# Kernel optimization log

Measured on AMD Instinct MI355X. Metric: run time of the kernel, lower is better.

## Reference

```python
import jax, jax.numpy as jnp
import numpy as np

B, T, D, P = 4, 2048, 1024, 128

def setup_inputs() -> dict:
    key = jax.random.key(0)
    ks = jax.random.split(key, 10)
    inp = {
        "x": jax.random.normal(ks[0], (B, T, D), dtype=jnp.float32),
        "Q_filt": jax.random.normal(ks[1], (P, P), dtype=jnp.float32),
        "K_filt": jax.random.normal(ks[2], (P, P), dtype=jnp.float32),
        "W_in": jax.random.normal(ks[3], (D, P), dtype=jnp.float32) / np.sqrt(D),
        "b_in": jax.random.normal(ks[4], (P,), dtype=jnp.float32) * 0.01,
        "W_v": jax.random.normal(ks[5], (D, P), dtype=jnp.float32) / np.sqrt(D),
        "b_v": jax.random.normal(ks[6], (P,), dtype=jnp.float32) * 0.01,
        "W_o": jax.random.normal(ks[7], (P, D), dtype=jnp.float32) / np.sqrt(P),
        "b_o": jax.random.normal(ks[8], (D,), dtype=jnp.float32) * 0.01,
        "decay": jnp.ones((T,), dtype=jnp.float32),
    }
    return inp

def reference(x, Q_filt, K_filt, W_in, b_in, W_v, b_v, W_o, b_o, decay):
    # x: (B,T,D)
    x_proj = x @ W_in + b_in          # (B,T,P)
    Q = x_proj @ Q_filt               # (B,T,P)
    K = x_proj @ K_filt               # (B,T,P)
    V = x @ W_v + b_v                 # (B,T,P)
    # outer-product state per timestep, scaled by per-step decay
    Z = jnp.einsum('bti,btj->btij', V, K) * decay[None, :, None, None]
    H = jnp.cumsum(Z, axis=1)         # (B,T,P,P) cumulative linear-attn state
    Y = jnp.einsum('bti,btij->btj', Q, H)  # (B,T,P)
    return Y @ W_o + b_o              # (B,T,D)
```

## Files before the change

### kernel.cpp

```cpp
#include <hip/hip_runtime.h>

#define BB 4
#define TT 2048
#define DD 1024
#define PP 128
#define NC 16
#define CH 128

typedef __attribute__((ext_vector_type(8))) short bf16x8;
typedef __attribute__((ext_vector_type(4))) float f32x4;

__device__ inline ushort f2bf(float f) {
  unsigned u = __builtin_bit_cast(unsigned, f);
  u = (u + 0x7FFF + ((u >> 16) & 1)) >> 16;
  return (ushort)u;
}

__device__ inline void gll16(const void* g, void* l) {
  __builtin_amdgcn_global_load_lds(
      (const __attribute__((address_space(1))) void*)g,
      (__attribute__((address_space(3))) void*)l, 16, 0, 0);
}

__device__ inline int swzoff(int row, int kbyte) {
  return row * 256 + (kbyte ^ ((row & 7) << 4));
}
__device__ inline int swz128(int row, int kbyte) {
  return row * 128 + (kbyte ^ ((row & 7) << 4));
}

template <int NI, int NT>
__device__ inline void stage_swz(const ushort* __restrict__ g, int ld, int koff,
                                 char* lds, int tid) {
#pragma unroll
  for (int j = 0; j < NI; ++j) {
    int L = j * (NT * 16) + tid * 16;
    int row = L >> 8;
    int off = (L & 255) ^ ((row & 7) << 4);
    gll16(g + (size_t)row * ld + koff + (off >> 1),
          lds + j * (NT * 16) + ((tid & (NT - 64)) << 4));
  }
}
template <int NI, int NT>
__device__ inline void stage_swz128(const ushort* __restrict__ g, int ld,
                                    int koff, char* lds, int tid) {
#pragma unroll
  for (int j = 0; j < NI; ++j) {
    int L = j * (NT * 16) + tid * 16;
    int row = L >> 7;
    int off = (L & 127) ^ ((row & 7) << 4);
    gll16(g + (size_t)row * ld + koff + (off >> 1),
          lds + j * (NT * 16) + ((tid & (NT - 64)) << 4));
  }
}

__device__ inline bf16x8 ld_swz(const char* lds, int row, int kbyte) {
  return *(const bf16x8*)(lds + swzoff(row, kbyte));
}
__device__ inline bf16x8 ld_swz128(const char* lds, int row, int kbyte) {
  return *(const bf16x8*)(lds + swz128(row, kbyte));
}

__device__ inline bf16x8 pack8(const float4& a, const float4& b) {
  bf16x8 v;
  v[0] = (short)f2bf(a.x); v[1] = (short)f2bf(a.y);
  v[2] = (short)f2bf(a.z); v[3] = (short)f2bf(a.w);
  v[4] = (short)f2bf(b.x); v[5] = (short)f2bf(b.y);
  v[6] = (short)f2bf(b.z); v[7] = (short)f2bf(b.w);
  return v;
}

__global__ __launch_bounds__(256) void prep_t(
    const float* __restrict__ Qf, const float* __restrict__ Kf,
    const float* __restrict__ W_in, const float* __restrict__ b_in,
    const float* __restrict__ W_v, const float* __restrict__ b_v,
    const float* __restrict__ W_o, ushort* __restrict__ WcatT,
    ushort* __restrict__ QKcT, ushort* __restrict__ WoT,
    float* __restrict__ bcat) {
  const int bid = blockIdx.x;
  const int t = threadIdx.x;
  if (bid == 104) {
    bcat[t] = (t < 128) ? b_in[t] : b_v[t - 128];
    return;
  }
  const float* src;
  ushort* dst;
  int ld_src, ld_dst, nn0;
  if (bid < 64) {
    int tn = bid >> 4, tk = bid & 15;
    src = (tn < 2) ? W_in : W_v;
    nn0 = (tn & 1) * 64;
    ld_src = 128;
    src += (size_t)(tk * 64) * 128;
    dst = WcatT + (size_t)(tn * 64) * 1024 + tk * 64;
    ld_dst = 1024;
  } else if (bid < 96) {
    int j = bid - 64, tn = j >> 1, tk = j & 1;
    src = W_o;
    nn0 = tn * 64;
    ld_src = 1024;
    src += (size_t)(tk * 64) * 1024;
    dst = WoT + (size_t)(tn * 64) * 128 + tk * 64;
    ld_dst = 128;
  } else {
    int j = bid - 96, tn = j >> 1, tk = j & 1;
    src = (tn < 2) ? Qf : Kf;
    nn0 = (tn & 1) * 64;
    ld_src = 128;
    src += (size_t)(tk * 64) * 128;
    dst = QKcT + (size_t)(tn * 64) * 128 + tk * 64;
    ld_dst = 128;
  }
  __shared__ ushort Tt[64][68];
  const int kr = t >> 4, nc = (t & 15) * 4;
#pragma unroll
  for (int p = 0; p < 4; ++p) {
    float4 v = *(const float4*)&src[(size_t)(p * 16 + kr) * ld_src + nn0 + nc];
    Tt[p * 16 + kr][nc + 0] = f2bf(v.x);
    Tt[p * 16 + kr][nc + 1] = f2bf(v.y);
    Tt[p * 16 + kr][nc + 2] = f2bf(v.z);
    Tt[p * 16 + kr][nc + 3] = f2bf(v.w);
  }
  __syncthreads();
  const int nr = t >> 4, kc = (t & 15) * 4;
#pragma unroll
  for (int p = 0; p < 4; ++p) {
    ushort4 o;
    o.x = Tt[kc + 0][p * 16 + nr];
    o.y = Tt[kc + 1][p * 16 + nr];
    o.z = Tt[kc + 2][p * 16 + nr];
    o.w = Tt[kc + 3][p * 16 + nr];
    *(ushort4*)&dst[(size_t)(p * 16 + nr) * ld_dst + kc] = o;
  }
}

__global__ __launch_bounds__(512, 4) void gemm_xw(
    const float* __restrict__ x, const ushort* __restrict__ WcatT,
    const float* __restrict__ bcat, ushort* __restrict__ XP,
    ushort* __restrict__ V, ushort* __restrict__ VT) {
  __shared__ char sm[2][24576];
  const int bid = blockIdx.x;
  const int swz = (bid & 7) * 32 + (bid >> 3);
  const int bm = (swz >> 1) * 64;
  const int bn = (swz & 1) * 128;
  const int tid = threadIdx.x, w = tid >> 6, l = tid & 63;
  const int wr = w >> 2, wc = w & 3, lr = l & 15, lk = l >> 4;

  const int arow = tid >> 3;
  const int acol = (tid & 7) * 8;
  const float* Ax = x + (size_t)(bm + arow) * DD + acol;
  const ushort* Bg = WcatT + (size_t)bn * DD;

  float4 ra[2];
  f32x4 z = {0.f, 0.f, 0.f, 0.f};
  f32x4 acc[2][2];
#pragma unroll
  for (int m = 0; m < 2; ++m)
#pragma unroll
    for (int n = 0; n < 2; ++n) acc[m][n] = z;

#define LOADA(t)                                                 \
  {                                                              \
    const float4* p = (const float4*)(Ax + (((t) & 15) << 6));   \
    ra[0] = p[0];                                                \
    ra[1] = p[1];                                                \
  }
#define WRITEA(lds) \
  { *(bf16x8*)((lds) + swz128(arow, acol * 2)) = pack8(ra[0], ra[1]); }

  LOADA(0);
  stage_swz128<2, 512>(Bg, DD, 0, sm[0] + 8192, tid);
  asm volatile("s_waitcnt vmcnt(2)" ::: "memory");
  WRITEA(sm[0]);
  LOADA(1);

  int cur = 0;
  for (int t = 0; t < 16; ++t) {
    char* nxt = sm[cur ^ 1];
    stage_swz128<2, 512>(Bg, DD, ((t + 1) & 15) << 6, nxt + 8192, tid);
    asm volatile("s_waitcnt vmcnt(2)" ::: "memory");
    WRITEA(nxt);
    LOADA(t + 2);
    asm volatile("s_waitcnt lgkmcnt(0)" ::: "memory");
    __builtin_amdgcn_s_barrier();
    const char* cp = sm[cur];
#pragma unroll
    for (int ks = 0; ks < 2; ++ks) {
      const int kb = ks * 64 + lk * 16;
      bf16x8 af[2], bfp[2];
#pragma unroll
      for (int m = 0; m < 2; ++m)
        af[m] = ld_swz128(cp, wr * 32 + m * 16 + lr, kb);
#pragma unroll
      for (int n = 0; n < 2; ++n)
        bfp[n] = ld_swz128(cp + 8192, wc * 32 + n * 16 + lr, kb);
#pragma unroll
      for (int m = 0; m < 2; ++m)
#pragma unroll
        for (int n = 0; n < 2; ++n)
          acc[m][n] = __builtin_amdgcn_mfma_f32_16x16x32_bf16(af[m], bfp[n], acc[m][n], 0, 0, 0);
    }
    __builtin_amdgcn_s_barrier();
    cur ^= 1;
  }
  asm volatile("s_waitcnt vmcnt(0)" ::: "memory");
#undef LOADA
#undef WRITEA

  if (bn == 0) {
#pragma unroll
    for (int m = 0; m < 2; ++m)
#pragma unroll
      for (int n = 0; n < 2; ++n) {
        const int rowb = bm + wr * 32 + m * 16 + lk * 4;
        const int col = wc * 32 + n * 16 + lr;
        const float bv = bcat[col];
#pragma unroll
        for (int j = 0; j < 4; ++j)
          XP[(size_t)(rowb + j) * PP + col] = f2bf(acc[m][n][j] + bv);
      }
  } else {
    ushort(*VTt)[72] = (ushort(*)[72]) & sm[0][0];
#pragma unroll
    for (int m = 0; m < 2; ++m)
#pragma unroll
      for (int n = 0; n < 2; ++n) {
        const int tl = wr * 32 + m * 16 + lk * 4;
        const int cc = wc * 32 + n * 16 + lr;
        const float bv = bcat[128 + cc];
#pragma unroll
        for (int j = 0; j < 4; ++j) {
          ushort u = f2bf(acc[m][n][j] + bv);
          V[(size_t)(bm + tl + j) * PP + cc] = u;
          VTt[cc][tl + j] = u;
        }
      }
    __syncthreads();
    const int row = tid >> 2;
#pragma unroll
    for (int i = 0; i < 2; ++i) {
      const int ch = (tid & 3) * 2 + i;
      bf16x8 v = *(const bf16x8*)&VTt[row][ch * 8];
      *(bf16x8*)&VT[(size_t)row * (BB * TT) + bm + ch * 8] = v;
    }
  }
}

__global__ __launch_bounds__(512, 4) void qk_state(
    const ushort* __restrict__ XP, const ushort* __restrict__ QKcT,
    const ushort* __restrict__ VT, const float* __restrict__ decay,
    ushort* __restrict__ Qb, ushort* __restrict__ KdT,
    float* __restrict__ Sc2) {
  __shared__ char sm[81920];
  char* smA = sm;
  char* smB = sm + 16384;
  const int blk = blockIdx.x;
  const int bc = blk >> 1, mh = blk & 1;
  const size_t r0 = (size_t)(bc >> 4) * TT + (bc & 15) * CH;
  const size_t rh = r0 + mh * 64;
  const int tid = threadIdx.x, w = tid >> 6, l = tid & 63;
  const int wr = w >> 2, wc = w & 3, lr = l & 15, lk = l >> 4;

  stage_swz<2, 512>(XP + rh * PP, PP, 0, smA, tid);
  stage_swz<8, 512>(QKcT, PP, 0, smB, tid);

  f32x4 z = {0.f, 0.f, 0.f, 0.f};
  f32x4 acc[2][4];
#pragma unroll
  for (int m = 0; m < 2; ++m)
#pragma unroll
    for (int n = 0; n < 4; ++n) acc[m][n] = z;
  __syncthreads();

#pragma unroll
  for (int ks = 0; ks < 4; ++ks) {
    const int kb = ks * 64 + lk * 16;
    bf16x8 af[2], bfp[4];
#pragma unroll
    for (int m = 0; m < 2; ++m) af[m] = ld_swz(smA, wr * 32 + m * 16 + lr, kb);
#pragma unroll
    for (int n = 0; n < 4; ++n)
      bfp[n] = ld_swz(smB, wc * 64 + n * 16 + lr, kb);
#pragma unroll
    for (int m = 0; m < 2; ++m)
#pragma unroll
      for (int n = 0; n < 4; ++n)
        acc[m][n] = __builtin_amdgcn_mfma_f32_16x16x32_bf16(af[m], bfp[n], acc[m][n], 0, 0, 0);
  }
  __syncthreads();

#pragma unroll
  for (int m = 0; m < 2; ++m)
#pragma unroll
    for (int n = 0; n < 4; ++n) {
      const int rowl = wr * 32 + m * 16 + lk * 4;
      const int col = wc * 64 + n * 16 + lr;
      if (col < 128) {
#pragma unroll
        for (int j = 0; j < 4; ++j)
          Qb[(rh + rowl + j) * PP + col] = f2bf(acc[m][n][j]);
      } else {
        const int cc = col - 128;
#pragma unroll
        for (int j = 0; j < 4; ++j) {
          float v = acc[m][n][j] * decay[(rh + rowl + j) & (TT - 1)];
          *(ushort*)(smA + swz128(cc, (rowl + j) * 2)) = f2bf(v);
        }
      }
    }
  __syncthreads();

  {
    const int cc = tid >> 2;
#pragma unroll
    for (int i = 0; i < 2; ++i) {
      const int ch = (tid & 3) * 2 + i;
      bf16x8 v = ld_swz128(smA, cc, ch * 16);
      *(bf16x8*)&KdT[(size_t)cc * (BB * TT) + rh + ch * 8] = v;
    }
  }

  f32x4 a2[4][2];
#pragma unroll
  for (int m = 0; m < 4; ++m)
#pragma unroll
    for (int n = 0; n < 2; ++n) a2[m][n] = z;
#pragma unroll
  for (int ks = 0; ks < 2; ++ks) {
    const int kb = ks * 64 + lk * 16;
    const int kk = ks * 32 + lk * 8;
    bf16x8 af[4], bfp[2];
#pragma unroll
    for (int m = 0; m < 4; ++m)
      af[m] = ld_swz128(smA, wr * 64 + m * 16 + lr, kb);
#pragma unroll
    for (int n = 0; n < 2; ++n)
      bfp[n] = *(const bf16x8*)&VT[(size_t)(wc * 32 + n * 16 + lr) * (BB * TT) + rh + kk];
#pragma unroll
    for (int m = 0; m < 4; ++m)
#pragma unroll
      for (int n = 0; n < 2; ++n)
        a2[m][n] = __builtin_amdgcn_mfma_f32_16x16x32_bf16(af[m], bfp[n], a2[m][n], 0, 0, 0);
  }
#pragma unroll
  for (int m = 0; m < 4; ++m)
#pragma unroll
    for (int n = 0; n < 2; ++n)
#pragma unroll
      for (int j = 0; j < 4; ++j)
        Sc2[((size_t)bc * 2 + mh) * 16384 +
            (size_t)(wr * 64 + m * 16 + lk * 4 + j) * 128 +
            (wc * 32 + n * 16 + lr)] = a2[m][n][j];
}

__global__ __launch_bounds__(256) void chunk_scan(const float* __restrict__ Sc2,
                                                  ushort* __restrict__ SxT) {
  const int b = blockIdx.y;
  const int e = blockIdx.x * 256 + threadIdx.x;
  float run = 0.f;
#pragma unroll
  for (int c = 0; c < NC; ++c) {
    const size_t bc = (size_t)(b * NC + c);
    SxT[bc * 16384 + e] = f2bf(run);
    run += Sc2[bc * 2 * 16384 + e] + Sc2[(bc * 2 + 1) * 16384 + e];
  }
}

__global__ __launch_bounds__(256) void attn_mfma(
    const ushort* __restrict__ Qb, const ushort* __restrict__ V,
    const ushort* __restrict__ KdT, const ushort* __restrict__ SxT,
    ushort* __restrict__ Y) {
  __shared__ char Am[64 * 256];
  const int blk = blockIdx.x;
  const int bc = blk >> 2, hr = (blk >> 1) & 1, hc = blk & 1;
  const int b = bc >> 4, c = bc & 15;
  const size_t r0 = (size_t)b * TT + c * CH;
  const int tid = threadIdx.x, w = tid >> 6, l = tid & 63;
  const int wr = w >> 1, wc = w & 1, lr = l & 15, lk = l >> 4;

  f32x4 z = {0.f, 0.f, 0.f, 0.f};
  f32x4 a1[2][4];
#pragma unroll
  for (int m = 0; m < 2; ++m)
#pragma unroll
    for (int n = 0; n < 4; ++n) a1[m][n] = z;

#pragma unroll
  for (int ks = 0; ks < 4; ++ks) {
    const int kk = ks * 32 + lk * 8;
    bf16x8 af[2], bf[4];
#pragma unroll
    for (int m = 0; m < 2; ++m)
      af[m] = *(const bf16x8*)&Qb[(r0 + hr * 64 + wr * 32 + m * 16 + lr) * 128 + kk];
#pragma unroll
    for (int n = 0; n < 4; ++n)
      bf[n] = *(const bf16x8*)&V[(r0 + wc * 64 + n * 16 + lr) * 128 + kk];
#pragma unroll
    for (int m = 0; m < 2; ++m)
#pragma unroll
      for (int n = 0; n < 4; ++n)
        a1[m][n] = __builtin_amdgcn_mfma_f32_16x16x32_bf16(af[m], bf[n], a1[m][n], 0, 0, 0);
  }
#pragma unroll
  for (int m = 0; m < 2; ++m)
#pragma unroll
    for (int n = 0; n < 4; ++n)
#pragma unroll
      for (int j = 0; j < 4; ++j) {
        int tl = wr * 32 + m * 16 + lk * 4 + j;
        int t = hr * 64 + tl;
        int s = wc * 64 + n * 16 + lr;
        float v = (s <= t) ? a1[m][n][j] : 0.f;
        *(ushort*)(Am + swzoff(tl, s * 2)) = f2bf(v);
      }
  __syncthreads();

  f32x4 a2[2][2];
#pragma unroll
  for (int m = 0; m < 2; ++m)
#pragma unroll
    for (int n = 0; n < 2; ++n) a2[m][n] = z;
#pragma unroll
  for (int ks = 0; ks < 4; ++ks) {
    const int kb = ks * 64 + lk * 16, kk = ks * 32 + lk * 8;
    bf16x8 af[2], bf[2];
#pragma unroll
    for (int m = 0; m < 2; ++m)
      af[m] = ld_swz(Am, wr * 32 + m * 16 + lr, kb);
#pragma unroll
    for (int n = 0; n < 2; ++n)
      bf[n] = *(const bf16x8*)&KdT[(size_t)(hc * 64 + wc * 32 + n * 16 + lr) * (BB * TT) + r0 + kk];
#pragma unroll
    for (int m = 0; m < 2; ++m)
#pragma unroll
      for (int n = 0; n < 2; ++n)
        a2[m][n] = __builtin_amdgcn_mfma_f32_16x16x32_bf16(af[m], bf[n], a2[m][n], 0, 0, 0);
  }
#pragma unroll
  for (int ks = 0; ks < 4; ++ks) {
    const int kk = ks * 32 + lk * 8;
    bf16x8 af[2], bf[2];
#pragma unroll
    for (int m = 0; m < 2; ++m)
      af[m] = *(const bf16x8*)&Qb[(r0 + hr * 64 + wr * 32 + m * 16 + lr) * 128 + kk];
#pragma unroll
    for (int n = 0; n < 2; ++n)
      bf[n] = *(const bf16x8*)&SxT[(size_t)bc * 16384 +
                                   (size_t)(hc * 64 + wc * 32 + n * 16 + lr) * 128 + kk];
#pragma unroll
    for (int m = 0; m < 2; ++m)
#pragma unroll
      for (int n = 0; n < 2; ++n)
        a2[m][n] = __builtin_amdgcn_mfma_f32_16x16x32_bf16(af[m], bf[n], a2[m][n], 0, 0, 0);
  }
#pragma unroll
  for (int m = 0; m < 2; ++m)
#pragma unroll
    for (int n = 0; n < 2; ++n)
#pragma unroll
      for (int j = 0; j < 4; ++j) {
        int t = hr * 64 + wr * 32 + m * 16 + lk * 4 + j;
        int col = hc * 64 + wc * 32 + n * 16 + lr;
        Y[(r0 + t) * 128 + col] = f2bf(a2[m][n][j]);
      }
}

__global__ __launch_bounds__(256) void gemm_out(
    const ushort* __restrict__ Y, const ushort* __restrict__ WoT,
    const float* __restrict__ b_o, float* __restrict__ out) {
  __shared__ char sm[49152];
  const int bid = blockIdx.x;
  const int swz = (bid & 7) * 128 + (bid >> 3);
  const int bm = (swz >> 3) * 64, bn = (swz & 7) * 128;
  const int tid = threadIdx.x, w = tid >> 6, l = tid & 63;
  const int wr = w >> 1, wc = w & 1, lr = l & 15, lk = l >> 4;
  stage_swz<4, 256>(Y + (size_t)bm * PP, PP, 0, sm, tid);
  stage_swz<8, 256>(WoT + (size_t)bn * PP, PP, 0, sm + 16384, tid);
  f32x4 z = {0.f, 0.f, 0.f, 0.f};
  f32x4 acc[2][4];
#pragma unroll
  for (int m = 0; m < 2; ++m)
#pragma unroll
    for (int n = 0; n < 4; ++n) acc[m][n] = z;
  __syncthreads();
#pragma unroll
  for (int ks = 0; ks < 4; ++ks) {
    const int kb = ks * 64 + lk * 16;
    bf16x8 af[2], bfp[4];
#pragma unroll
    for (int m = 0; m < 2; ++m) af[m] = ld_swz(sm, wr * 32 + m * 16 + lr, kb);
#pragma unroll
    for (int n = 0; n < 4; ++n)
      bfp[n] = ld_swz(sm + 16384, wc * 64 + n * 16 + lr, kb);
#pragma unroll
    for (int m = 0; m < 2; ++m)
#pragma unroll
      for (int n = 0; n < 4; ++n)
        acc[m][n] = __builtin_amdgcn_mfma_f32_16x16x32_bf16(af[m], bfp[n], acc[m][n], 0, 0, 0);
  }
#pragma unroll
  for (int m = 0; m < 2; ++m)
#pragma unroll
    for (int n = 0; n < 4; ++n) {
      const int rowb = bm + wr * 32 + m * 16 + lk * 4;
      const int col = bn + wc * 64 + n * 16 + lr;
      const float bv = b_o[col];
#pragma unroll
      for (int j = 0; j < 4; ++j)
        out[(size_t)(rowb + j) * DD + col] = acc[m][n][j] + bv;
    }
}

extern "C" void kernel_launch(void* const* d_in, const int* in_sizes, int n_in,
                              void* d_out, int out_size, void* d_ws, size_t ws_size,
                              hipStream_t stream) {
  const float* x = (const float*)d_in[0];
  const float* Qf = (const float*)d_in[1];
  const float* Kf = (const float*)d_in[2];
  const float* W_in = (const float*)d_in[3];
  const float* b_in = (const float*)d_in[4];
  const float* W_v = (const float*)d_in[5];
  const float* b_v = (const float*)d_in[6];
  const float* W_o = (const float*)d_in[7];
  const float* b_o = (const float*)d_in[8];
  const float* decay = (const float*)d_in[9];
  float* out = (float*)d_out;
  char* W = (char*)d_ws;

  ushort* XP    = (ushort*)(W);
  ushort* V     = (ushort*)(W + 2097152);
  ushort* VT    = (ushort*)(W + 4194304);
  ushort* Qb    = (ushort*)(W + 6291456);
  ushort* KdT   = (ushort*)(W + 8388608);
  float*  Sc2   = (float*)(W + 10485760);
  ushort* SxT   = (ushort*)(W + 18874368);
  ushort* Yb    = (ushort*)(W + 20971520);
  ushort* WcatT = (ushort*)(W + 23068672);
  ushort* QKcT  = (ushort*)(W + 23592960);
  ushort* WoT   = (ushort*)(W + 23658496);
  float*  bcat  = (float*)(W + 23920640);

  prep_t<<<105, 256, 0, stream>>>(Qf, Kf, W_in, b_in, W_v, b_v, W_o,
                                  WcatT, QKcT, WoT, bcat);
  gemm_xw<<<256, 512, 0, stream>>>(x, WcatT, bcat, XP, V, VT);
  qk_state<<<2 * BB * NC, 512, 0, stream>>>(XP, QKcT, VT, decay, Qb, KdT, Sc2);
  chunk_scan<<<dim3(64, BB), 256, 0, stream>>>(Sc2, SxT);
  attn_mfma<<<4 * BB * NC, 256, 0, stream>>>(Qb, V, KdT, SxT, Yb);
  gemm_out<<<1024, 256, 0, stream>>>(Yb, WoT, b_o, out);
}
```

Measured before the change: 50.99 us.

## Fuse output projection into attention kernel, keeping Y tile in LDS

The attention kernel and the separate output GEMM are merged into one kernel. Each block now computes a full 64-row by 128-column Y tile (instead of a 64x64 half), stores it swizzled in shared memory, and multiplies it directly by W_o over a 512-column half of the output. This removes one kernel launch and the global write and reload of the bf16 Y intermediate. In exchange, the output projection runs on only 256 blocks instead of 1024, reading W_o straight from global memory with higher register use. The Q@S and causal parts are now computed twice, once per column half (hc).

```diff
diff --git a/kernel.cpp b/kernel.cpp
--- a/kernel.cpp
+++ b/kernel.cpp
@@ -366,32 +366,35 @@
   }
 }
 
-__global__ __launch_bounds__(256) void attn_mfma(
+__global__ __launch_bounds__(256) void attn_out(
     const ushort* __restrict__ Qb, const ushort* __restrict__ V,
     const ushort* __restrict__ KdT, const ushort* __restrict__ SxT,
-    ushort* __restrict__ Y) {
+    const ushort* __restrict__ WoT, const float* __restrict__ b_o,
+    float* __restrict__ out) {
   __shared__ char Am[64 * 256];
+  __shared__ char Yl[64 * 256];
   const int blk = blockIdx.x;
   const int bc = blk >> 2, hr = (blk >> 1) & 1, hc = blk & 1;
   const int b = bc >> 4, c = bc & 15;
   const size_t r0 = (size_t)b * TT + c * CH;
+  const size_t gr0 = r0 + hr * 64;
   const int tid = threadIdx.x, w = tid >> 6, l = tid & 63;
   const int wr = w >> 1, wc = w & 1, lr = l & 15, lk = l >> 4;
 
   f32x4 z = {0.f, 0.f, 0.f, 0.f};
+
   f32x4 a1[2][4];
 #pragma unroll
   for (int m = 0; m < 2; ++m)
 #pragma unroll
     for (int n = 0; n < 4; ++n) a1[m][n] = z;
-
 #pragma unroll
   for (int ks = 0; ks < 4; ++ks) {
     const int kk = ks * 32 + lk * 8;
     bf16x8 af[2], bf[4];
 #pragma unroll
     for (int m = 0; m < 2; ++m)
-      af[m] = *(const bf16x8*)&Qb[(r0 + hr * 64 + wr * 32 + m * 16 + lr) * 128 + kk];
+      af[m] = *(const bf16x8*)&Qb[(gr0 + wr * 32 + m * 16 + lr) * 128 + kk];
 #pragma unroll
     for (int n = 0; n < 4; ++n)
       bf[n] = *(const bf16x8*)&V[(r0 + wc * 64 + n * 16 + lr) * 128 + kk];
@@ -415,100 +418,92 @@
       }
   __syncthreads();
 
-  f32x4 a2[2][2];
-#pragma unroll
-  for (int m = 0; m < 2; ++m)
-#pragma unroll
-    for (int n = 0; n < 2; ++n) a2[m][n] = z;
+  f32x4 a2[2][4];
+#pragma unroll
+  for (int m = 0; m < 2; ++m)
+#pragma unroll
+    for (int n = 0; n < 4; ++n) a2[m][n] = z;
 #pragma unroll
   for (int ks = 0; ks < 4; ++ks) {
     const int kb = ks * 64 + lk * 16, kk = ks * 32 + lk * 8;
-    bf16x8 af[2], bf[2];
+    bf16x8 af[2], bf[4];
 #pragma unroll
     for (int m = 0; m < 2; ++m)
       af[m] = ld_swz(Am, wr * 32 + m * 16 + lr, kb);
 #pragma unroll
-    for (int n = 0; n < 2; ++n)
-      bf[n] = *(const bf16x8*)&KdT[(size_t)(hc * 64 + wc * 32 + n * 16 + lr) * (BB * TT) + r0 + kk];
-#pragma unroll
-    for (int m = 0; m < 2; ++m)
-#pragma unroll
-      for (int n = 0; n < 2; ++n)
+    for (int n = 0; n < 4; ++n)
+      bf[n] = *(const bf16x8*)&KdT[(size_t)(wc * 64 + n * 16 + lr) * (BB * TT) + r0 + kk];
+#pragma unroll
+    for (int m = 0; m < 2; ++m)
+#pragma unroll
+      for (int n = 0; n < 4; ++n)
         a2[m][n] = __builtin_amdgcn_mfma_f32_16x16x32_bf16(af[m], bf[n], a2[m][n], 0, 0, 0);
   }
 #pragma unroll
   for (int ks = 0; ks < 4; ++ks) {
     const int kk = ks * 32 + lk * 8;
-    bf16x8 af[2], bf[2];
-#pragma unroll
-    for (int m = 0; m < 2; ++m)
-      af[m] = *(const bf16x8*)&Qb[(r0 + hr * 64 + wr * 32 + m * 16 + lr) * 128 + kk];
-#pragma unroll
-    for (int n = 0; n < 2; ++n)
+    bf16x8 af[2], bf[4];
+#pragma unroll
+    for (int m = 0; m < 2; ++m)
+      af[m] = *(const bf16x8*)&Qb[(gr0 + wr * 32 + m * 16 + lr) * 128 + kk];
+#pragma unroll
+    for (int n = 0; n < 4; ++n)
       bf[n] = *(const bf16x8*)&SxT[(size_t)bc * 16384 +
-                                   (size_t)(hc * 64 + wc * 32 + n * 16 + lr) * 128 + kk];
-#pragma unroll
-    for (int m = 0; m < 2; ++m)
-#pragma unroll
-      for (int n = 0; n < 2; ++n)
+                                   (size_t)(wc * 64 + n * 16 + lr) * 128 + kk];
+#pragma unroll
+    for (int m = 0; m < 2; ++m)
+#pragma unroll
+      for (int n = 0; n < 4; ++n)
         a2[m][n] = __builtin_amdgcn_mfma_f32_16x16x32_bf16(af[m], bf[n], a2[m][n], 0, 0, 0);
   }
 #pragma unroll
   for (int m = 0; m < 2; ++m)
 #pragma unroll
-    for (int n = 0; n < 2; ++n)
+    for (int n = 0; n < 4; ++n)
 #pragma unroll
       for (int j = 0; j < 4; ++j) {
-        int t = hr * 64 + wr * 32 + m * 16 + lk * 4 + j;
-        int col = hc * 64 + wc * 32 + n * 16 + lr;
-        Y[(r0 + t) * 128 + col] = f2bf(a2[m][n][j]);
+        int tl = wr * 32 + m * 16 + lk * 4 + j;
+        int s = wc * 64 + n * 16 + lr;
+        *(ushort*)(Yl + swzoff(tl, s * 2)) = f2bf(a2[m][n][j]);
       }
-}
-
-__global__ __launch_bounds__(256) void gemm_out(
-    const ushort* __restrict__ Y, const ushort* __restrict__ WoT,
-    const float* __restrict__ b_o, float* __restrict__ out) {
-  __shared__ char sm[49152];
-  const int bid = blockIdx.x;
-  const int swz = (bid & 7) * 128 + (bid >> 3);
-  const int bm = (swz >> 3) * 64, bn = (swz & 7) * 128;
-  const int tid = threadIdx.x, w = tid >> 6, l = tid & 63;
-  const int wr = w >> 1, wc = w & 1, lr = l & 15, lk = l >> 4;
-  stage_swz<4, 256>(Y + (size_t)bm * PP, PP, 0, sm, tid);
-  stage_swz<8, 256>(WoT + (size_t)bn * PP, PP, 0, sm + 16384, tid);
-  f32x4 z = {0.f, 0.f, 0.f, 0.f};
-  f32x4 acc[2][4];
-#pragma unroll
-  for (int m = 0; m < 2; ++m)
-#pragma unroll
-    for (int n = 0; n < 4; ++n) acc[m][n] = z;
   __syncthreads();
-#pragma unroll
-  for (int ks = 0; ks < 4; ++ks) {
-    const int kb = ks * 64 + lk * 16;
-    bf16x8 af[2], bfp[4];
-#pragma unroll
-    for (int m = 0; m < 2; ++m) af[m] = ld_swz(sm, wr * 32 + m * 16 + lr, kb);
-#pragma unroll
-    for (int n = 0; n < 4; ++n)
-      bfp[n] = ld_swz(sm + 16384, wc * 64 + n * 16 + lr, kb);
-#pragma unroll
-    for (int m = 0; m < 2; ++m)
-#pragma unroll
-      for (int n = 0; n < 4; ++n)
-        acc[m][n] = __builtin_amdgcn_mfma_f32_16x16x32_bf16(af[m], bfp[n], acc[m][n], 0, 0, 0);
-  }
-#pragma unroll
-  for (int m = 0; m < 2; ++m)
-#pragma unroll
-    for (int n = 0; n < 4; ++n) {
-      const int rowb = bm + wr * 32 + m * 16 + lk * 4;
-      const int col = bn + wc * 64 + n * 16 + lr;
-      const float bv = b_o[col];
-#pragma unroll
-      for (int j = 0; j < 4; ++j)
-        out[(size_t)(rowb + j) * DD + col] = acc[m][n][j] + bv;
+
+#pragma unroll
+  for (int np = 0; np < 2; ++np) {
+    const int col0 = hc * 512 + np * 256 + wc * 128;
+    f32x4 a3[2][8];
+#pragma unroll
+    for (int m = 0; m < 2; ++m)
+#pragma unroll
+      for (int n = 0; n < 8; ++n) a3[m][n] = z;
+#pragma unroll
+    for (int ks = 0; ks < 4; ++ks) {
+      const int kb = ks * 64 + lk * 16, kk = ks * 32 + lk * 8;
+      bf16x8 af[2], bf[8];
+#pragma unroll
+      for (int m = 0; m < 2; ++m)
+        af[m] = ld_swz(Yl, wr * 32 + m * 16 + lr, kb);
+#pragma unroll
+      for (int n = 0; n < 8; ++n)
+        bf[n] = *(const bf16x8*)&WoT[(size_t)(col0 + n * 16 + lr) * 128 + kk];
+#pragma unroll
+      for (int m = 0; m < 2; ++m)
+#pragma unroll
+        for (int n = 0; n < 8; ++n)
+          a3[m][n] = __builtin_amdgcn_mfma_f32_16x16x32_bf16(af[m], bf[n], a3[m][n], 0, 0, 0);
     }
+#pragma unroll
+    for (int m = 0; m < 2; ++m)
+#pragma unroll
+      for (int n = 0; n < 8; ++n) {
+        const int rowb = (int)(gr0 + wr * 32 + m * 16 + lk * 4);
+        const int col = col0 + n * 16 + lr;
+        const float bv = b_o[col];
+#pragma unroll
+        for (int j = 0; j < 4; ++j)
+          out[(size_t)(rowb + j) * DD + col] = a3[m][n][j] + bv;
+      }
+  }
 }
 
 extern "C" void kernel_launch(void* const* d_in, const int* in_sizes, int n_in,
@@ -534,17 +529,15 @@
   ushort* KdT   = (ushort*)(W + 8388608);
   float*  Sc2   = (float*)(W + 10485760);
   ushort* SxT   = (ushort*)(W + 18874368);
-  ushort* Yb    = (ushort*)(W + 20971520);
-  ushort* WcatT = (ushort*)(W + 23068672);
-  ushort* QKcT  = (ushort*)(W + 23592960);
-  ushort* WoT   = (ushort*)(W + 23658496);
-  float*  bcat  = (float*)(W + 23920640);
+  ushort* WcatT = (ushort*)(W + 20971520);
+  ushort* QKcT  = (ushort*)(W + 21495808);
+  ushort* WoT   = (ushort*)(W + 21561344);
+  float*  bcat  = (float*)(W + 21823488);
 
   prep_t<<<105, 256, 0, stream>>>(Qf, Kf, W_in, b_in, W_v, b_v, W_o,
                                   WcatT, QKcT, WoT, bcat);
   gemm_xw<<<256, 512, 0, stream>>>(x, WcatT, bcat, XP, V, VT);
   qk_state<<<2 * BB * NC, 512, 0, stream>>>(XP, QKcT, VT, decay, Qb, KdT, Sc2);
   chunk_scan<<<dim3(64, BB), 256, 0, stream>>>(Sc2, SxT);
-  attn_mfma<<<4 * BB * NC, 256, 0, stream>>>(Qb, V, KdT, SxT, Yb);
-  gemm_out<<<1024, 256, 0, stream>>>(Yb, WoT, b_o, out);
-}
+  attn_out<<<4 * BB * NC, 256, 0, stream>>>(Qb, V, KdT, SxT, WoT, b_o, out);
+}
```

New measurement: 60.01 us. 1.18x slower.

## Split qk_state into Q and K halves across more blocks with XCD-aware mapping

Applied to the files above, without the earlier changes.

qk_state now launches 256 blocks of 256 threads instead of 128 blocks of 512. Each (chunk, half-row) unit is split so one block computes the Q projection and a sibling block computes the decayed K projection plus the K^T V chunk state, which spreads work over more CUs. Block indices in both qk_state and attn_mfma are remapped so blocks on the same XCD handle nearby chunks, aiming for better L2 locality. The cost is that the XP tile is staged twice and each K-half block does twice the state MFMA work with more accumulator registers.

```diff
diff --git a/kernel.cpp b/kernel.cpp
--- a/kernel.cpp
+++ b/kernel.cpp
@@ -246,23 +246,26 @@
   }
 }
 
-__global__ __launch_bounds__(512, 4) void qk_state(
+__global__ __launch_bounds__(256) void qk_state(
     const ushort* __restrict__ XP, const ushort* __restrict__ QKcT,
     const ushort* __restrict__ VT, const float* __restrict__ decay,
     ushort* __restrict__ Qb, ushort* __restrict__ KdT,
     float* __restrict__ Sc2) {
-  __shared__ char sm[81920];
+  __shared__ char sm[49152];
   char* smA = sm;
   char* smB = sm + 16384;
-  const int blk = blockIdx.x;
-  const int bc = blk >> 1, mh = blk & 1;
+  const int p = blockIdx.x;
+  const int xcd = p & 7, idx = p >> 3;
+  const int unit = xcd + 8 * (idx >> 1);
+  const int half = idx & 1;
+  const int bc = unit >> 1, mh = unit & 1;
   const size_t r0 = (size_t)(bc >> 4) * TT + (bc & 15) * CH;
   const size_t rh = r0 + mh * 64;
   const int tid = threadIdx.x, w = tid >> 6, l = tid & 63;
-  const int wr = w >> 2, wc = w & 3, lr = l & 15, lk = l >> 4;
-
-  stage_swz<2, 512>(XP + rh * PP, PP, 0, smA, tid);
-  stage_swz<8, 512>(QKcT, PP, 0, smB, tid);
+  const int wr = w >> 1, wc = w & 1, lr = l & 15, lk = l >> 4;
+
+  stage_swz<4, 256>(XP + rh * PP, PP, 0, smA, tid);
+  stage_swz<8, 256>(QKcT + (size_t)half * 128 * PP, PP, 0, smB, tid);
 
   f32x4 z = {0.f, 0.f, 0.f, 0.f};
   f32x4 acc[2][4];
@@ -287,70 +290,77 @@
       for (int n = 0; n < 4; ++n)
         acc[m][n] = __builtin_amdgcn_mfma_f32_16x16x32_bf16(af[m], bfp[n], acc[m][n], 0, 0, 0);
   }
+
+  if (half == 0) {
+#pragma unroll
+    for (int m = 0; m < 2; ++m)
+#pragma unroll
+      for (int n = 0; n < 4; ++n) {
+        const int rowl = wr * 32 + m * 16 + lk * 4;
+        const int col = wc * 64 + n * 16 + lr;
+#pragma unroll
+        for (int j = 0; j < 4; ++j)
+          Qb[(rh + rowl + j) * PP + col] = f2bf(acc[m][n][j]);
+      }
+    return;
+  }
+
   __syncthreads();
-
 #pragma unroll
   for (int m = 0; m < 2; ++m)
 #pragma unroll
     for (int n = 0; n < 4; ++n) {
       const int rowl = wr * 32 + m * 16 + lk * 4;
-      const int col = wc * 64 + n * 16 + lr;
-      if (col < 128) {
-#pragma unroll
-        for (int j = 0; j < 4; ++j)
-          Qb[(rh + rowl + j) * PP + col] = f2bf(acc[m][n][j]);
-      } else {
-        const int cc = col - 128;
-#pragma unroll
-        for (int j = 0; j < 4; ++j) {
-          float v = acc[m][n][j] * decay[(rh + rowl + j) & (TT - 1)];
-          *(ushort*)(smA + swz128(cc, (rowl + j) * 2)) = f2bf(v);
-        }
+      const int cc = wc * 64 + n * 16 + lr;
+#pragma unroll
+      for (int j = 0; j < 4; ++j) {
+        float v = acc[m][n][j] * decay[(rh + rowl + j) & (TT - 1)];
+        *(ushort*)(smA + swz128(cc, (rowl + j) * 2)) = f2bf(v);
       }
     }
   __syncthreads();
 
   {
-    const int cc = tid >> 2;
-#pragma unroll
-    for (int i = 0; i < 2; ++i) {
-      const int ch = (tid & 3) * 2 + i;
+    const int cc = tid >> 1;
+#pragma unroll
+    for (int i = 0; i < 4; ++i) {
+      const int ch = (tid & 1) * 4 + i;
       bf16x8 v = ld_swz128(smA, cc, ch * 16);
       *(bf16x8*)&KdT[(size_t)cc * (BB * TT) + rh + ch * 8] = v;
     }
   }
 
-  f32x4 a2[4][2];
+  f32x4 a2[4][4];
 #pragma unroll
   for (int m = 0; m < 4; ++m)
 #pragma unroll
-    for (int n = 0; n < 2; ++n) a2[m][n] = z;
+    for (int n = 0; n < 4; ++n) a2[m][n] = z;
 #pragma unroll
   for (int ks = 0; ks < 2; ++ks) {
     const int kb = ks * 64 + lk * 16;
     const int kk = ks * 32 + lk * 8;
-    bf16x8 af[4], bfp[2];
+    bf16x8 af[4], bfp[4];
 #pragma unroll
     for (int m = 0; m < 4; ++m)
       af[m] = ld_swz128(smA, wr * 64 + m * 16 + lr, kb);
 #pragma unroll
-    for (int n = 0; n < 2; ++n)
-      bfp[n] = *(const bf16x8*)&VT[(size_t)(wc * 32 + n * 16 + lr) * (BB * TT) + rh + kk];
+    for (int n = 0; n < 4; ++n)
+      bfp[n] = *(const bf16x8*)&VT[(size_t)(wc * 64 + n * 16 + lr) * (BB * TT) + rh + kk];
 #pragma unroll
     for (int m = 0; m < 4; ++m)
 #pragma unroll
-      for (int n = 0; n < 2; ++n)
+      for (int n = 0; n < 4; ++n)
         a2[m][n] = __builtin_amdgcn_mfma_f32_16x16x32_bf16(af[m], bfp[n], a2[m][n], 0, 0, 0);
   }
 #pragma unroll
   for (int m = 0; m < 4; ++m)
 #pragma unroll
-    for (int n = 0; n < 2; ++n)
+    for (int n = 0; n < 4; ++n)
 #pragma unroll
       for (int j = 0; j < 4; ++j)
-        Sc2[((size_t)bc * 2 + mh) * 16384 +
+        Sc2[(size_t)unit * 16384 +
             (size_t)(wr * 64 + m * 16 + lk * 4 + j) * 128 +
-            (wc * 32 + n * 16 + lr)] = a2[m][n][j];
+            (wc * 64 + n * 16 + lr)] = a2[m][n][j];
 }
 
 __global__ __launch_bounds__(256) void chunk_scan(const float* __restrict__ Sc2,
@@ -371,8 +381,11 @@
     const ushort* __restrict__ KdT, const ushort* __restrict__ SxT,
     ushort* __restrict__ Y) {
   __shared__ char Am[64 * 256];
-  const int blk = blockIdx.x;
-  const int bc = blk >> 2, hr = (blk >> 1) & 1, hc = blk & 1;
+  const int p = blockIdx.x;
+  const int xcd = p & 7, idx = p >> 3;
+  const int bc = xcd + 8 * (idx >> 2);
+  const int q = idx & 3;
+  const int hr = q >> 1, hc = q & 1;
   const int b = bc >> 4, c = bc & 15;
   const size_t r0 = (size_t)b * TT + c * CH;
   const int tid = threadIdx.x, w = tid >> 6, l = tid & 63;
@@ -543,7 +556,7 @@
   prep_t<<<105, 256, 0, stream>>>(Qf, Kf, W_in, b_in, W_v, b_v, W_o,
                                   WcatT, QKcT, WoT, bcat);
   gemm_xw<<<256, 512, 0, stream>>>(x, WcatT, bcat, XP, V, VT);
-  qk_state<<<2 * BB * NC, 512, 0, stream>>>(XP, QKcT, VT, decay, Qb, KdT, Sc2);
+  qk_state<<<256, 256, 0, stream>>>(XP, QKcT, VT, decay, Qb, KdT, Sc2);
   chunk_scan<<<dim3(64, BB), 256, 0, stream>>>(Sc2, SxT);
   attn_mfma<<<4 * BB * NC, 256, 0, stream>>>(Qb, V, KdT, SxT, Yb);
   gemm_out<<<1024, 256, 0, stream>>>(Yb, WoT, b_o, out);
```

Result: faster. 49.43 us (-3.1%).

## Fuse Q/K filter GEMM into input projection and split chunk-state kernel

Applied to the files above, without the earlier changes.

The Q/K filter projection is folded into the epilogue of gemm_xw for the bn==0 blocks, so x_proj stays in LDS and never goes to global memory. A new chunk_state kernel computes one full 128x128 chunk state per chunk, split into four quadrant blocks, which removes the two-half partial sums that chunk_scan had to add. Block indices in chunk_state and attn_mfma are remapped so that blocks sharing a chunk land on the same XCD. The cost is an unbalanced gemm_xw: half its blocks do extra MFMA work, use more LDS and lose the occupancy hint of 4.

```diff
diff --git a/kernel.cpp b/kernel.cpp
--- a/kernel.cpp
+++ b/kernel.cpp
@@ -134,11 +134,13 @@
   }
 }
 
-__global__ __launch_bounds__(512, 4) void gemm_xw(
+__global__ __launch_bounds__(512) void gemm_xw(
     const float* __restrict__ x, const ushort* __restrict__ WcatT,
-    const float* __restrict__ bcat, ushort* __restrict__ XP,
-    ushort* __restrict__ V, ushort* __restrict__ VT) {
-  __shared__ char sm[2][24576];
+    const ushort* __restrict__ QKcT, const float* __restrict__ bcat,
+    const float* __restrict__ decay, ushort* __restrict__ Qb,
+    ushort* __restrict__ KdT, ushort* __restrict__ V,
+    ushort* __restrict__ VT) {
+  __shared__ char sm[81920];
   const int bid = blockIdx.x;
   const int swz = (bid & 7) * 32 + (bid >> 3);
   const int bm = (swz >> 1) * 64;
@@ -169,21 +171,21 @@
   { *(bf16x8*)((lds) + swz128(arow, acol * 2)) = pack8(ra[0], ra[1]); }
 
   LOADA(0);
-  stage_swz128<2, 512>(Bg, DD, 0, sm[0] + 8192, tid);
+  stage_swz128<2, 512>(Bg, DD, 0, sm + 8192, tid);
   asm volatile("s_waitcnt vmcnt(2)" ::: "memory");
-  WRITEA(sm[0]);
+  WRITEA(sm);
   LOADA(1);
 
   int cur = 0;
   for (int t = 0; t < 16; ++t) {
-    char* nxt = sm[cur ^ 1];
+    char* nxt = sm + (cur ^ 1) * 24576;
     stage_swz128<2, 512>(Bg, DD, ((t + 1) & 15) << 6, nxt + 8192, tid);
     asm volatile("s_waitcnt vmcnt(2)" ::: "memory");
     WRITEA(nxt);
     LOADA(t + 2);
     asm volatile("s_waitcnt lgkmcnt(0)" ::: "memory");
     __builtin_amdgcn_s_barrier();
-    const char* cp = sm[cur];
+    const char* cp = sm + cur * 24576;
 #pragma unroll
     for (int ks = 0; ks < 2; ++ks) {
       const int kb = ks * 64 + lk * 16;
@@ -204,6 +206,7 @@
     cur ^= 1;
   }
   asm volatile("s_waitcnt vmcnt(0)" ::: "memory");
+  __syncthreads();
 #undef LOADA
 #undef WRITEA
 
@@ -212,15 +215,71 @@
     for (int m = 0; m < 2; ++m)
 #pragma unroll
       for (int n = 0; n < 2; ++n) {
-        const int rowb = bm + wr * 32 + m * 16 + lk * 4;
+        const int rowl = wr * 32 + m * 16 + lk * 4;
         const int col = wc * 32 + n * 16 + lr;
         const float bv = bcat[col];
 #pragma unroll
         for (int j = 0; j < 4; ++j)
-          XP[(size_t)(rowb + j) * PP + col] = f2bf(acc[m][n][j] + bv);
+          *(ushort*)(sm + swzoff(rowl + j, col * 2)) = f2bf(acc[m][n][j] + bv);
       }
+    stage_swz<8, 512>(QKcT, PP, 0, sm + 16384, tid);
+    __syncthreads();
+
+    f32x4 a2[2][4];
+#pragma unroll
+    for (int m = 0; m < 2; ++m)
+#pragma unroll
+      for (int n = 0; n < 4; ++n) a2[m][n] = z;
+#pragma unroll
+    for (int ks = 0; ks < 4; ++ks) {
+      const int kb = ks * 64 + lk * 16;
+      bf16x8 af[2], bfp[4];
+#pragma unroll
+      for (int m = 0; m < 2; ++m)
+        af[m] = ld_swz(sm, wr * 32 + m * 16 + lr, kb);
+#pragma unroll
+      for (int n = 0; n < 4; ++n)
+        bfp[n] = ld_swz(sm + 16384, wc * 64 + n * 16 + lr, kb);
+#pragma unroll
+      for (int m = 0; m < 2; ++m)
+#pragma unroll
+        for (int n = 0; n < 4; ++n)
+          a2[m][n] = __builtin_amdgcn_mfma_f32_16x16x32_bf16(af[m], bfp[n], a2[m][n], 0, 0, 0);
+    }
+    __syncthreads();
+
+#pragma unroll
+    for (int m = 0; m < 2; ++m)
+#pragma unroll
+      for (int n = 0; n < 4; ++n) {
+        const int rowl = wr * 32 + m * 16 + lk * 4;
+        const int col = wc * 64 + n * 16 + lr;
+        if (col < 128) {
+#pragma unroll
+          for (int j = 0; j < 4; ++j)
+            Qb[(size_t)(bm + rowl + j) * PP + col] = f2bf(a2[m][n][j]);
+        } else {
+          const int cc = col - 128;
+#pragma unroll
+          for (int j = 0; j < 4; ++j) {
+            float v = a2[m][n][j] * decay[(bm + rowl + j) & (TT - 1)];
+            *(ushort*)(sm + swz128(cc, (rowl + j) * 2)) = f2bf(v);
+          }
+        }
+      }
+    __syncthreads();
+
+    {
+      const int cc = tid >> 2;
+#pragma unroll
+      for (int i = 0; i < 2; ++i) {
+        const int ch = (tid & 3) * 2 + i;
+        bf16x8 v = ld_swz128(sm, cc, ch * 16);
+        *(bf16x8*)&KdT[(size_t)cc * (BB * TT) + bm + ch * 8] = v;
+      }
+    }
   } else {
-    ushort(*VTt)[72] = (ushort(*)[72]) & sm[0][0];
+    ushort(*VTt)[72] = (ushort(*)[72]) & sm[0];
 #pragma unroll
     for (int m = 0; m < 2; ++m)
 #pragma unroll
@@ -246,123 +305,61 @@
   }
 }
 
-__global__ __launch_bounds__(512, 4) void qk_state(
-    const ushort* __restrict__ XP, const ushort* __restrict__ QKcT,
-    const ushort* __restrict__ VT, const float* __restrict__ decay,
-    ushort* __restrict__ Qb, ushort* __restrict__ KdT,
-    float* __restrict__ Sc2) {
-  __shared__ char sm[81920];
-  char* smA = sm;
-  char* smB = sm + 16384;
-  const int blk = blockIdx.x;
-  const int bc = blk >> 1, mh = blk & 1;
+__global__ __launch_bounds__(256) void chunk_state(
+    const ushort* __restrict__ KdT, const ushort* __restrict__ VT,
+    float* __restrict__ Sc) {
+  const int p = blockIdx.x;
+  const int xcd = p & 7, idx = p >> 3;
+  const int bc = xcd + 8 * (idx >> 2);
+  const int q = idx & 3;
+  const int qj = q >> 1, qi = q & 1;
   const size_t r0 = (size_t)(bc >> 4) * TT + (bc & 15) * CH;
-  const size_t rh = r0 + mh * 64;
   const int tid = threadIdx.x, w = tid >> 6, l = tid & 63;
-  const int wr = w >> 2, wc = w & 3, lr = l & 15, lk = l >> 4;
-
-  stage_swz<2, 512>(XP + rh * PP, PP, 0, smA, tid);
-  stage_swz<8, 512>(QKcT, PP, 0, smB, tid);
+  const int wr = w >> 1, wc = w & 1, lr = l & 15, lk = l >> 4;
 
   f32x4 z = {0.f, 0.f, 0.f, 0.f};
-  f32x4 acc[2][4];
-#pragma unroll
-  for (int m = 0; m < 2; ++m)
-#pragma unroll
-    for (int n = 0; n < 4; ++n) acc[m][n] = z;
-  __syncthreads();
-
+  f32x4 acc[2][2];
+#pragma unroll
+  for (int m = 0; m < 2; ++m)
+#pragma unroll
+    for (int n = 0; n < 2; ++n) acc[m][n] = z;
 #pragma unroll
   for (int ks = 0; ks < 4; ++ks) {
-    const int kb = ks * 64 + lk * 16;
-    bf16x8 af[2], bfp[4];
-#pragma unroll
-    for (int m = 0; m < 2; ++m) af[m] = ld_swz(smA, wr * 32 + m * 16 + lr, kb);
-#pragma unroll
-    for (int n = 0; n < 4; ++n)
-      bfp[n] = ld_swz(smB, wc * 64 + n * 16 + lr, kb);
-#pragma unroll
-    for (int m = 0; m < 2; ++m)
-#pragma unroll
-      for (int n = 0; n < 4; ++n)
-        acc[m][n] = __builtin_amdgcn_mfma_f32_16x16x32_bf16(af[m], bfp[n], acc[m][n], 0, 0, 0);
-  }
-  __syncthreads();
-
-#pragma unroll
-  for (int m = 0; m < 2; ++m)
-#pragma unroll
-    for (int n = 0; n < 4; ++n) {
-      const int rowl = wr * 32 + m * 16 + lk * 4;
-      const int col = wc * 64 + n * 16 + lr;
-      if (col < 128) {
-#pragma unroll
-        for (int j = 0; j < 4; ++j)
-          Qb[(rh + rowl + j) * PP + col] = f2bf(acc[m][n][j]);
-      } else {
-        const int cc = col - 128;
-#pragma unroll
-        for (int j = 0; j < 4; ++j) {
-          float v = acc[m][n][j] * decay[(rh + rowl + j) & (TT - 1)];
-          *(ushort*)(smA + swz128(cc, (rowl + j) * 2)) = f2bf(v);
-        }
-      }
-    }
-  __syncthreads();
-
-  {
-    const int cc = tid >> 2;
-#pragma unroll
-    for (int i = 0; i < 2; ++i) {
-      const int ch = (tid & 3) * 2 + i;
-      bf16x8 v = ld_swz128(smA, cc, ch * 16);
-      *(bf16x8*)&KdT[(size_t)cc * (BB * TT) + rh + ch * 8] = v;
-    }
-  }
-
-  f32x4 a2[4][2];
-#pragma unroll
-  for (int m = 0; m < 4; ++m)
-#pragma unroll
-    for (int n = 0; n < 2; ++n) a2[m][n] = z;
-#pragma unroll
-  for (int ks = 0; ks < 2; ++ks) {
-    const int kb = ks * 64 + lk * 16;
     const int kk = ks * 32 + lk * 8;
-    bf16x8 af[4], bfp[2];
-#pragma unroll
-    for (int m = 0; m < 4; ++m)
-      af[m] = ld_swz128(smA, wr * 64 + m * 16 + lr, kb);
+    bf16x8 af[2], bf[2];
+#pragma unroll
+    for (int m = 0; m < 2; ++m)
+      af[m] = *(const bf16x8*)&KdT[(size_t)(qj * 64 + wr * 32 + m * 16 + lr) * (BB * TT) + r0 + kk];
 #pragma unroll
     for (int n = 0; n < 2; ++n)
-      bfp[n] = *(const bf16x8*)&VT[(size_t)(wc * 32 + n * 16 + lr) * (BB * TT) + rh + kk];
-#pragma unroll
-    for (int m = 0; m < 4; ++m)
+      bf[n] = *(const bf16x8*)&VT[(size_t)(qi * 64 + wc * 32 + n * 16 + lr) * (BB * TT) + r0 + kk];
+#pragma unroll
+    for (int m = 0; m < 2; ++m)
 #pragma unroll
       for (int n = 0; n < 2; ++n)
-        a2[m][n] = __builtin_amdgcn_mfma_f32_16x16x32_bf16(af[m], bfp[n], a2[m][n], 0, 0, 0);
-  }
-#pragma unroll
-  for (int m = 0; m < 4; ++m)
+        acc[m][n] = __builtin_amdgcn_mfma_f32_16x16x32_bf16(af[m], bf[n], acc[m][n], 0, 0, 0);
+  }
+#pragma unroll
+  for (int m = 0; m < 2; ++m)
 #pragma unroll
     for (int n = 0; n < 2; ++n)
 #pragma unroll
       for (int j = 0; j < 4; ++j)
-        Sc2[((size_t)bc * 2 + mh) * 16384 +
-            (size_t)(wr * 64 + m * 16 + lk * 4 + j) * 128 +
-            (wc * 32 + n * 16 + lr)] = a2[m][n][j];
-}
-
-__global__ __launch_bounds__(256) void chunk_scan(const float* __restrict__ Sc2,
+        Sc[(size_t)bc * 16384 +
+           (size_t)(qj * 64 + wr * 32 + m * 16 + lk * 4 + j) * 128 +
+           (qi * 64 + wc * 32 + n * 16 + lr)] = acc[m][n][j];
+}
+
+__global__ __launch_bounds__(256) void chunk_scan(const float* __restrict__ Sc,
                                                   ushort* __restrict__ SxT) {
   const int b = blockIdx.y;
   const int e = blockIdx.x * 256 + threadIdx.x;
   float run = 0.f;
 #pragma unroll
   for (int c = 0; c < NC; ++c) {
-    const size_t bc = (size_t)(b * NC + c);
-    SxT[bc * 16384 + e] = f2bf(run);
-    run += Sc2[bc * 2 * 16384 + e] + Sc2[(bc * 2 + 1) * 16384 + e];
+    const size_t idx = (size_t)(b * NC + c) * 16384 + e;
+    SxT[idx] = f2bf(run);
+    run += Sc[idx];
   }
 }
 
@@ -371,10 +368,12 @@
     const ushort* __restrict__ KdT, const ushort* __restrict__ SxT,
     ushort* __restrict__ Y) {
   __shared__ char Am[64 * 256];
-  const int blk = blockIdx.x;
-  const int bc = blk >> 2, hr = (blk >> 1) & 1, hc = blk & 1;
-  const int b = bc >> 4, c = bc & 15;
-  const size_t r0 = (size_t)b * TT + c * CH;
+  const int p = blockIdx.x;
+  const int xcd = p & 7, idx = p >> 3;
+  const int bc = xcd + 8 * (idx >> 2);
+  const int q = idx & 3;
+  const int hr = q >> 1, hc = q & 1;
+  const size_t r0 = (size_t)(bc >> 4) * TT + (bc & 15) * CH;
   const int tid = threadIdx.x, w = tid >> 6, l = tid & 63;
   const int wr = w >> 1, wc = w & 1, lr = l & 15, lk = l >> 4;
 
@@ -527,24 +526,24 @@
   float* out = (float*)d_out;
   char* W = (char*)d_ws;
 
-  ushort* XP    = (ushort*)(W);
-  ushort* V     = (ushort*)(W + 2097152);
-  ushort* VT    = (ushort*)(W + 4194304);
-  ushort* Qb    = (ushort*)(W + 6291456);
-  ushort* KdT   = (ushort*)(W + 8388608);
-  float*  Sc2   = (float*)(W + 10485760);
-  ushort* SxT   = (ushort*)(W + 18874368);
-  ushort* Yb    = (ushort*)(W + 20971520);
-  ushort* WcatT = (ushort*)(W + 23068672);
-  ushort* QKcT  = (ushort*)(W + 23592960);
-  ushort* WoT   = (ushort*)(W + 23658496);
-  float*  bcat  = (float*)(W + 23920640);
+  ushort* V     = (ushort*)(W);
+  ushort* VT    = (ushort*)(W + 2097152);
+  ushort* Qb    = (ushort*)(W + 4194304);
+  ushort* KdT   = (ushort*)(W + 6291456);
+  float*  Sc    = (float*)(W + 8388608);
+  ushort* SxT   = (ushort*)(W + 12582912);
+  ushort* Yb    = (ushort*)(W + 14680064);
+  ushort* WcatT = (ushort*)(W + 16777216);
+  ushort* QKcT  = (ushort*)(W + 17301504);
+  ushort* WoT   = (ushort*)(W + 17367040);
+  float*  bcat  = (float*)(W + 17629184);
 
   prep_t<<<105, 256, 0, stream>>>(Qf, Kf, W_in, b_in, W_v, b_v, W_o,
                                   WcatT, QKcT, WoT, bcat);
-  gemm_xw<<<256, 512, 0, stream>>>(x, WcatT, bcat, XP, V, VT);
-  qk_state<<<2 * BB * NC, 512, 0, stream>>>(XP, QKcT, VT, decay, Qb, KdT, Sc2);
-  chunk_scan<<<dim3(64, BB), 256, 0, stream>>>(Sc2, SxT);
-  attn_mfma<<<4 * BB * NC, 256, 0, stream>>>(Qb, V, KdT, SxT, Yb);
+  gemm_xw<<<256, 512, 0, stream>>>(x, WcatT, QKcT, bcat, decay,
+                                   Qb, KdT, V, VT);
+  chunk_state<<<256, 256, 0, stream>>>(KdT, VT, Sc);
+  chunk_scan<<<dim3(64, BB), 256, 0, stream>>>(Sc, SxT);
+  attn_mfma<<<256, 256, 0, stream>>>(Qb, V, KdT, SxT, Yb);
   gemm_out<<<1024, 256, 0, stream>>>(Yb, WoT, b_o, out);
 }
```

After: 48.78 us. -4.3%, faster.
